# Performance work log

Measured on AMD Instinct MI355X. Metric: run time of the kernel, lower is better.

## Reference

```python
import jax, jax.numpy as jnp
import numpy as np

EPS = 1e-6  # EPS[torch.float32]
B, N = 4096, 64
MAX_ITER = 5


def setup_inputs() -> dict:
    key = jax.random.key(0)
    x = jax.random.normal(key, (B, N, N), dtype=jnp.float32)
    # SPD input, as assumed by the matrix-log layer (EEG covariance-like)
    M = x @ jnp.swapaxes(x, -1, -2) / N + 1e-3 * jnp.eye(N, dtype=jnp.float32)
    return {"input": M}


def _qr_algorithm(A, max_iter=MAX_ITER):
    # 5 iterations of the batched QR eigen-iteration, as in the torch source
    n = A.shape[-1]
    eye = jnp.broadcast_to(jnp.eye(n, dtype=A.dtype), A.shape)

    def body(carry, _):
        A_k, Q_total = carry
        Q, R = jnp.linalg.qr(A_k)
        return (R @ Q, Q_total @ Q), None

    (A_k, Q_total), _ = jax.lax.scan(body, (A, eye), None, length=max_iter)
    s = jnp.diagonal(A_k, axis1=-2, axis2=-1)  # approx eigenvalues [B, n]
    return s, Q_total  # Q_total: approx eigenvectors [B, n, n]


def reference(input):
    s, U = _qr_algorithm(input)
    smod = jnp.log(jnp.clip(s, EPS))  # sym_logm.value: clamp then log
    # U @ diag(smod) @ U^T, without materializing diag_embed
    X = (U * smod[..., None, :]) @ jnp.swapaxes(U, -1, -2)
    return X
```

## Files before the change

### kernel.cpp

```cpp
#include <hip/hip_runtime.h>
#include <math.h>

#define N 64
#define GS 68
#define MAX_ITER 5

__device__ __forceinline__ float rl(float x, int lane) {
    return __uint_as_float(__builtin_amdgcn_readlane(__float_as_uint(x), lane));
}

__global__ __launch_bounds__(64, 2) void logm_kernel(const float* __restrict__ gin,
                                                     float* __restrict__ gout) {
    __shared__ __align__(16) float G[N * GS];
    const int t = threadIdx.x;
    const long b = blockIdx.x;
    const float* __restrict__ in = gin + b * (long)(N * N);
    float* __restrict__ out = gout + b * (long)(N * N);

    float a[N], r[N], qt[N];

    #pragma unroll
    for (int i = 0; i < N; ++i) a[i] = in[i * N + t];
    #pragma unroll
    for (int i = 0; i < N; ++i) qt[i] = (i == t) ? 1.0f : 0.0f;

    float betaS = 0.f, v0S = 0.f, alS = 0.f;

    for (int iter = 0; iter < MAX_ITER; ++iter) {
        float dotA, dotQ, wA, wQ;
        {
            float dA0 = 0.f, dA1 = 0.f, dQ0 = 0.f, dQ1 = 0.f;
            #pragma unroll
            for (int i = 0; i < N; ++i) {
                const float c = rl(a[i], 0);
                if (i & 1) { dA1 = fmaf(c, a[i], dA1); dQ1 = fmaf(c, qt[i], dQ1); }
                else       { dA0 = fmaf(c, a[i], dA0); dQ0 = fmaf(c, qt[i], dQ0); }
            }
            dotA = dA0 + dA1; dotQ = dQ0 + dQ1;
            wA = a[0]; wQ = qt[0];
        }

        #pragma unroll
        for (int kb = 0; kb < 8; ++kb) {
            const int dkEnd = (kb == 7) ? 7 : 8;
            for (int dk = 0; dk < dkEnd; ++dk) {
                const int k = 8 * kb + dk;
                const int k1 = k + 1;
                const float ss = rl(dotA, k);
                const float x0 = rl(wA, k);
                const float nrm = sqrtf(ss);
                const float alpha = (x0 >= 0.f) ? -nrm : nrm;
                const float v0 = x0 - alpha;
                const float vtv = fmaf(v0, v0, ss - x0 * x0);
                const float beta = (vtv > 1e-30f) ? __fdividef(2.0f, vtv) : 0.f;
                const float ca = beta * fmaf(-alpha, wA, dotA);
                const float cq = beta * fmaf(-alpha, wQ, dotQ);
                const float caE = (t > k) ? ca : 0.f;
                betaS = (t == k) ? beta  : betaS;
                v0S   = (t == k) ? v0    : v0S;
                alS   = (t == k) ? alpha : alS;

                float nA0 = 0.f, nA1 = 0.f, nQ0 = 0.f, nQ1 = 0.f, nwA = 0.f, nwQ = 0.f;
                #pragma unroll
                for (int i0 = 8 * kb; i0 < N; i0 += 8) {
                    #pragma unroll
                    for (int u = 0; u < 8; ++u) {
                        const int i = i0 + u;
                        float cu = rl(a[i], k);
                        if (i0 == 8 * kb) cu = (i > k) ? cu : ((i == k) ? v0 : 0.f);
                        a[i]  = fmaf(-caE, cu, a[i]);
                        qt[i] = fmaf(-cq,  cu, qt[i]);
                        float c2 = rl(a[i], k1);
                        if (i0 == 8 * kb) c2 = (i > k) ? c2 : 0.f;
                        if (u & 1) { nA1 = fmaf(c2, a[i], nA1); nQ1 = fmaf(c2, qt[i], nQ1); }
                        else       { nA0 = fmaf(c2, a[i], nA0); nQ0 = fmaf(c2, qt[i], nQ0); }
                        if ((i0 == 8 * kb && u > 0) || (kb < 7 && i0 == 8 * kb + 8 && u == 0)) {
                            const bool e = (i == k1);
                            nwA = e ? a[i]  : nwA;
                            nwQ = e ? qt[i] : nwQ;
                        }
                    }
                }
                dotA = nA0 + nA1; dotQ = nQ0 + nQ1; wA = nwA; wQ = nwQ;
            }
        }

        #pragma unroll
        for (int i = 0; i < N; i += 4) {
            float4 w; w.x = a[i]; w.y = a[i + 1]; w.z = a[i + 2]; w.w = a[i + 3];
            *reinterpret_cast<float4*>(&G[t * GS + i]) = w;
        }
        G[t * GS + t] = (t == N - 1) ? a[N - 1] : alS;

        float dR, wRv;
        {
            float d0 = 0.f, d1 = 0.f;
            #pragma unroll
            for (int j = 0; j < N; ++j) {
                const float g = G[j * GS + t];
                const float rj = (j >= t) ? g : 0.f;
                r[j] = rj;
                a[j] = (j == t) ? v0S : ((j < t) ? 0.f : a[j]);
                const float c = rl(a[j], 0);
                if (j & 1) d1 = fmaf(c, rj, d1); else d0 = fmaf(c, rj, d0);
            }
            dR = d0 + d1; wRv = 0.f; (void)wRv;
        }

        for (int k = 0; k < N - 1; ++k) {
            const int k1 = k + 1;
            const float cc = rl(betaS, k) * dR;
            float nD0 = 0.f, nD1 = 0.f;
            #pragma unroll
            for (int i0 = 0; i0 < N; i0 += 8) {
                if (i0 + 8 > k) {
                    #pragma unroll
                    for (int u = 0; u < 8; ++u) {
                        const int j = i0 + u;
                        const float cu = rl(a[j], k);
                        r[j] = fmaf(-cc, cu, r[j]);
                        const float c2 = rl(a[j], k1);
                        if (u & 1) nD1 = fmaf(c2, r[j], nD1);
                        else       nD0 = fmaf(c2, r[j], nD0);
                    }
                }
            }
            dR = nD0 + nD1;
        }
        #pragma unroll
        for (int j = 0; j < N; ++j) a[j] = r[j];
    }

    #pragma unroll
    for (int l = 0; l < N; ++l) {
        const float dl = rl(a[l], l);
        const float sml = __logf(fmaxf(dl, 1e-6f));
        a[l] = sml * qt[l];
    }
    #pragma unroll
    for (int l = 0; l < N; l += 4) {
        float4 w; w.x = qt[l]; w.y = qt[l + 1]; w.z = qt[l + 2]; w.w = qt[l + 3];
        *reinterpret_cast<float4*>(&G[t * GS + l]) = w;
    }
    #pragma unroll 2
    for (int j = 0; j < N; ++j) {
        float e0 = 0.f, e1 = 0.f, e2 = 0.f, e3 = 0.f;
        #pragma unroll
        for (int l = 0; l < N; l += 4) {
            float4 u4 = *reinterpret_cast<const float4*>(&G[j * GS + l]);
            e0 = fmaf(a[l + 0], u4.x, e0);
            e1 = fmaf(a[l + 1], u4.y, e1);
            e2 = fmaf(a[l + 2], u4.z, e2);
            e3 = fmaf(a[l + 3], u4.w, e3);
        }
        out[j * N + t] = (e0 + e1) + (e2 + e3);
    }
}

extern "C" void kernel_launch(void* const* d_in, const int* in_sizes, int n_in,
                              void* d_out, int out_size, void* d_ws, size_t ws_size,
                              hipStream_t stream) {
    const float* in = (const float*)d_in[0];
    float* out = (float*)d_out;
    const int batch = in_sizes[0] / (N * N);
    hipLaunchKernelGGL(logm_kernel, dim3(batch), dim3(64), 0, stream, in, out);
}
```

Before: 1.398 ms.

## Stage Householder vectors in swizzled LDS and free the register array during R·Q

The Householder vectors are now written to shared memory with an XOR-free rotating swizzle instead of a padded layout. The R·Q application phase reads them as broadcast float4 loads from LDS rather than through readlane on the per-thread register array `a`. This removes two readlanes per element per step and the need to keep `a` live alongside `r`, which lowers register pressure. The launch bound is raised to three blocks per SIMD to gain occupancy, at the risk of register spilling.

```diff
diff --git a/kernel.cpp b/kernel.cpp
--- a/kernel.cpp
+++ b/kernel.cpp
@@ -2,16 +2,15 @@
 #include <math.h>
 
 #define N 64
-#define GS 68
 #define MAX_ITER 5
 
 __device__ __forceinline__ float rl(float x, int lane) {
     return __uint_as_float(__builtin_amdgcn_readlane(__float_as_uint(x), lane));
 }
 
-__global__ __launch_bounds__(64, 2) void logm_kernel(const float* __restrict__ gin,
+__global__ __launch_bounds__(64, 3) void logm_kernel(const float* __restrict__ gin,
                                                      float* __restrict__ gout) {
-    __shared__ __align__(16) float G[N * GS];
+    __shared__ __align__(16) float G[N * N];
     const int t = threadIdx.x;
     const long b = blockIdx.x;
     const float* __restrict__ in = gin + b * (long)(N * N);
@@ -85,26 +84,31 @@
             }
         }
 
+        const float diagR = (t == N - 1) ? a[N - 1] : alS;
         #pragma unroll
-        for (int i = 0; i < N; i += 4) {
-            float4 w; w.x = a[i]; w.y = a[i + 1]; w.z = a[i + 2]; w.w = a[i + 3];
-            *reinterpret_cast<float4*>(&G[t * GS + i]) = w;
+        for (int j = 0; j < N; j += 4) {
+            float4 w; w.x = a[j]; w.y = a[j + 1]; w.z = a[j + 2]; w.w = a[j + 3];
+            *reinterpret_cast<float4*>(&G[(t << 6) + ((j + (t << 2)) & 63)]) = w;
         }
-        G[t * GS + t] = (t == N - 1) ? a[N - 1] : alS;
+        G[(t << 6) + ((5 * t) & 63)] = v0S;
 
-        float dR, wRv;
+        float dR;
         {
+            #pragma unroll
+            for (int j = 0; j < N; ++j) {
+                const float g = G[(j << 6) + ((t + (j << 2)) & 63)];
+                r[j] = (j > t) ? g : ((j == t) ? diagR : 0.f);
+            }
             float d0 = 0.f, d1 = 0.f;
             #pragma unroll
-            for (int j = 0; j < N; ++j) {
-                const float g = G[j * GS + t];
-                const float rj = (j >= t) ? g : 0.f;
-                r[j] = rj;
-                a[j] = (j == t) ? v0S : ((j < t) ? 0.f : a[j]);
-                const float c = rl(a[j], 0);
-                if (j & 1) d1 = fmaf(c, rj, d1); else d0 = fmaf(c, rj, d0);
+            for (int j = 0; j < N; j += 4) {
+                const float4 v = *reinterpret_cast<const float4*>(&G[j]);
+                d0 = fmaf(v.x, r[j],     d0);
+                d1 = fmaf(v.y, r[j + 1], d1);
+                d0 = fmaf(v.z, r[j + 2], d0);
+                d1 = fmaf(v.w, r[j + 3], d1);
             }
-            dR = d0 + d1; wRv = 0.f; (void)wRv;
+            dR = d0 + d1;
         }
 
         for (int k = 0; k < N - 1; ++k) {
@@ -112,16 +116,29 @@
             const float cc = rl(betaS, k) * dR;
             float nD0 = 0.f, nD1 = 0.f;
             #pragma unroll
-            for (int i0 = 0; i0 < N; i0 += 8) {
-                if (i0 + 8 > k) {
+            for (int j0 = 0; j0 < N; j0 += 8) {
+                if (j0 + 8 > k) {
                     #pragma unroll
-                    for (int u = 0; u < 8; ++u) {
-                        const int j = i0 + u;
-                        const float cu = rl(a[j], k);
-                        r[j] = fmaf(-cc, cu, r[j]);
-                        const float c2 = rl(a[j], k1);
-                        if (u & 1) nD1 = fmaf(c2, r[j], nD1);
-                        else       nD0 = fmaf(c2, r[j], nD0);
+                    for (int h = 0; h < 2; ++h) {
+                        const int jc = j0 + 4 * h;
+                        float4 vk  = *reinterpret_cast<const float4*>(
+                            &G[(k  << 6) + ((jc + (k  << 2)) & 63)]);
+                        float4 vk1 = *reinterpret_cast<const float4*>(
+                            &G[(k1 << 6) + ((jc + (k1 << 2)) & 63)]);
+                        if (jc <= k) {
+                            vk.x  = (jc + 0 >= k)  ? vk.x  : 0.f;
+                            vk.y  = (jc + 1 >= k)  ? vk.y  : 0.f;
+                            vk.z  = (jc + 2 >= k)  ? vk.z  : 0.f;
+                            vk.w  = (jc + 3 >= k)  ? vk.w  : 0.f;
+                            vk1.x = (jc + 0 >= k1) ? vk1.x : 0.f;
+                            vk1.y = (jc + 1 >= k1) ? vk1.y : 0.f;
+                            vk1.z = (jc + 2 >= k1) ? vk1.z : 0.f;
+                            vk1.w = (jc + 3 >= k1) ? vk1.w : 0.f;
+                        }
+                        r[jc + 0] = fmaf(-cc, vk.x, r[jc + 0]); nD0 = fmaf(vk1.x, r[jc + 0], nD0);
+                        r[jc + 1] = fmaf(-cc, vk.y, r[jc + 1]); nD1 = fmaf(vk1.y, r[jc + 1], nD1);
+                        r[jc + 2] = fmaf(-cc, vk.z, r[jc + 2]); nD0 = fmaf(vk1.z, r[jc + 2], nD0);
+                        r[jc + 3] = fmaf(-cc, vk.w, r[jc + 3]); nD1 = fmaf(vk1.w, r[jc + 3], nD1);
                     }
                 }
             }
@@ -140,14 +157,15 @@
     #pragma unroll
     for (int l = 0; l < N; l += 4) {
         float4 w; w.x = qt[l]; w.y = qt[l + 1]; w.z = qt[l + 2]; w.w = qt[l + 3];
-        *reinterpret_cast<float4*>(&G[t * GS + l]) = w;
+        *reinterpret_cast<float4*>(&G[(t << 6) + ((l + (t << 2)) & 63)]) = w;
     }
     #pragma unroll 2
     for (int j = 0; j < N; ++j) {
         float e0 = 0.f, e1 = 0.f, e2 = 0.f, e3 = 0.f;
         #pragma unroll
         for (int l = 0; l < N; l += 4) {
-            float4 u4 = *reinterpret_cast<const float4*>(&G[j * GS + l]);
+            const float4 u4 = *reinterpret_cast<const float4*>(
+                &G[(j << 6) + ((l + (j << 2)) & 63)]);
             e0 = fmaf(a[l + 0], u4.x, e0);
             e1 = fmaf(a[l + 1], u4.y, e1);
             e2 = fmaf(a[l + 2], u4.z, e2);
```

Result: slower. 1.684 ms (+20.5%).
